# Kernel optimization log

Hardware: AMD Instinct MI355X
Metric: run time of the kernel (lower is better)

The kernel has to match this reference:

```python
import jax, jax.numpy as jnp
import numpy as np
from jax import lax

NUM_CLASSES = 5
NUM_TASKS = 20
CONV_CHANS = [(64, 3), (64, 64), (128, 64), (128, 128), (256, 128), (256, 256)]  # (out, in)


def setup_inputs() -> dict:
    key = jax.random.key(0)
    ks = jax.random.split(key, 16)
    B = 512
    x = jax.random.normal(ks[0], (B, 3, 32, 32), dtype=jnp.float32)
    tid = jax.random.randint(ks[1], (B,), 0, NUM_TASKS)
    inp = {"x": x, "tid": tid}
    for i, (oc, ic) in enumerate(CONV_CHANS):
        fan_in = ic * 9
        inp[f"w{i}"] = jax.random.normal(ks[2 + 2 * i], (oc, ic, 3, 3), dtype=jnp.float32) * np.float32((2.0 / fan_in) ** 0.5)
        inp[f"b{i}"] = jnp.zeros((oc,), dtype=jnp.float32)
    inp["cw"] = jax.random.normal(ks[14], (NUM_CLASSES * NUM_TASKS, 4096), dtype=jnp.float32) * np.float32(4096 ** -0.5)
    inp["cb"] = jnp.zeros((NUM_CLASSES * NUM_TASKS,), dtype=jnp.float32)
    return inp


def _conv_relu(x, w, b):
    y = lax.conv_general_dilated(x, w, window_strides=(1, 1), padding='SAME',
                                 dimension_numbers=('NCHW', 'OIHW', 'NCHW'))
    return jax.nn.relu(y + b[None, :, None, None])


def _maxpool2(x):
    return lax.reduce_window(x, -jnp.inf, lax.max, (1, 1, 2, 2), (1, 1, 2, 2), 'VALID')


def _forward(x, tid, ws, bs, cw, cb):
    # VGG cfg [64,64,'M',128,128,'M',256,256,'M']
    h = _conv_relu(x, ws[0], bs[0])
    h = _conv_relu(h, ws[1], bs[1])
    h = _maxpool2(h)
    h = _conv_relu(h, ws[2], bs[2])
    h = _conv_relu(h, ws[3], bs[3])
    h = _maxpool2(h)
    h = _conv_relu(h, ws[4], bs[4])
    h = _conv_relu(h, ws[5], bs[5])
    h = _maxpool2(h)                      # [B, 256, 4, 4]
    feat = h.reshape(h.shape[0], -1)      # [B, 4096], matches torch NCHW flatten
    # Batched task-indexed classifier: gather each sample's 5-row weight block.
    w_sel = cw.reshape(NUM_TASKS, NUM_CLASSES, 4096)[tid]   # [B, 5, 4096]
    b_sel = cb.reshape(NUM_TASKS, NUM_CLASSES)[tid]         # [B, 5]
    return jnp.einsum('bcd,bd->bc', w_sel, feat) + b_sel


def reference(x, tid, w0, b0, w1, b1, w2, b2, w3, b3, w4, b4, w5, b5, cw, cb):
    ws = (w0, w1, w2, w3, w4, w5)
    bs = (b0, b1, b2, b3, b4, b5)
    return _forward(x, tid, ws, bs, cw, cb)
```

## Files before the change

kernel.cpp:

```cpp
#include <hip/hip_runtime.h>


typedef __attribute__((ext_vector_type(8))) short short8;
typedef __attribute__((ext_vector_type(4))) float floatx4;
typedef unsigned int uint;
typedef unsigned short ushort;

__device__ __forceinline__ ushort f2bf(float f) {
    uint u = __float_as_uint(f);
    return (ushort)((u + 0x7fffu + ((u >> 16) & 1u)) >> 16);
}
__device__ __forceinline__ float bf2f(ushort h) {
    return __uint_as_float(((uint)h) << 16);
}

typedef const __attribute__((address_space(1))) unsigned int* gas_ptr;
typedef __attribute__((address_space(3))) unsigned int* las_ptr;
__device__ __forceinline__ void gload_lds16(const void* g, void* l) {
    __builtin_amdgcn_global_load_lds((gas_ptr)g, (las_ptr)l, 16, 0, 0);
}

__device__ __forceinline__ void wlin_one(
    const float* __restrict__ src, short* __restrict__ dst, int OC, int IC, int o)
{
    int j    = o & 7;
    int lane = (o >> 3) & 63;
    int r    = o >> 9;
    int G16  = OC >> 4;
    int g    = r % G16;  r /= G16;
    int kk   = r % 9;
    int icb  = r / 9;
    int oc = g * 16 + (lane & 15);
    int ic = icb * 32 + (lane >> 4) * 8 + j;
    dst[o] = (short)f2bf(src[((long)oc * IC + ic) * 9 + kk]);
}

#define N_W0 2048
#define N_W1 36864
#define N_W2 73728
#define N_W3 147456
#define N_W4 294912
#define N_W5 589824
#define N_CWB (100 * 4096)
#define N_WT_TOTAL (N_W0 + N_W1 + N_W2 + N_W3 + N_W4 + N_W5)
#define N_ALL (N_WT_TOTAL + N_CWB)

__global__ __launch_bounds__(256) void wtransform_all(
    const float* __restrict__ w0, const float* __restrict__ w1,
    const float* __restrict__ w2, const float* __restrict__ w3,
    const float* __restrict__ w4, const float* __restrict__ w5,
    const float* __restrict__ cw,
    short* __restrict__ wt0, short* __restrict__ wts1, short* __restrict__ wts2,
    short* __restrict__ wts3, short* __restrict__ wts4, short* __restrict__ wts5,
    short* __restrict__ zp, short* __restrict__ cwb)
{
    if (blockIdx.x == 0 && threadIdx.x < 32) zp[threadIdx.x] = 0;
    int idx = blockIdx.x * 256 + threadIdx.x;
    if (idx < N_W0) {
        int oc = idx >> 5, k = idx & 31;
        wt0[idx] = (k < 27) ? (short)f2bf(w0[oc * 27 + k]) : (short)0;
        return;
    }
    idx -= N_W0;
    if (idx < N_W1) { wlin_one(w1, wts1, 64, 64, idx); return; }
    idx -= N_W1;
    if (idx < N_W2) { wlin_one(w2, wts2, 128, 64, idx); return; }
    idx -= N_W2;
    if (idx < N_W3) { wlin_one(w3, wts3, 128, 128, idx); return; }
    idx -= N_W3;
    if (idx < N_W4) { wlin_one(w4, wts4, 256, 128, idx); return; }
    idx -= N_W4;
    if (idx < N_W5) { wlin_one(w5, wts5, 256, 256, idx); return; }
    idx -= N_W5;
    if (idx < N_CWB) cwb[idx] = (short)f2bf(cw[idx]);
}

__global__ __launch_bounds__(256, 2) void conv0_mfma(
    const float* __restrict__ x, const short* __restrict__ wT0,
    const float* __restrict__ b0, ushort* __restrict__ out)
{
    __shared__ float  s_x[3 * 18 * 34];
    __shared__ ushort s_b[4 * 512 * 8];

    const int tid  = threadIdx.x;
    const int wv   = tid >> 6;
    const int lane = tid & 63;
    const int quad = lane >> 4;
    const int l16  = lane & 15;
    const int b    = blockIdx.x >> 1;
    const int r0   = (blockIdx.x & 1) * 16;

    for (int idx = tid; idx < 3 * 18 * 34; idx += 256) {
        int c   = idx / 612;
        int rem = idx - c * 612;
        int ry  = rem / 34, rx = rem - ry * 34;
        int gy  = r0 + ry - 1, gx = rx - 1;
        float v = 0.f;
        if (gy >= 0 && gy < 32 && gx >= 0 && gx < 32)
            v = x[(((long)b * 3 + c) * 32 + gy) * 32 + gx];
        s_x[idx] = v;
    }
    __syncthreads();

#pragma unroll
    for (int rep = 0; rep < 2; ++rep) {
        int pxl = rep * 256 + tid;
        int py = pxl >> 5, px = pxl & 31;
        ushort v[32];
#pragma unroll
        for (int c = 0; c < 3; ++c)
#pragma unroll
            for (int ky = 0; ky < 3; ++ky)
#pragma unroll
                for (int kx = 0; kx < 3; ++kx)
                    v[c * 9 + ky * 3 + kx] = f2bf(s_x[c * 612 + (py + ky) * 34 + (px + kx)]);
#pragma unroll
        for (int k = 27; k < 32; ++k) v[k] = 0;
#pragma unroll
        for (int q = 0; q < 4; ++q)
            *(uint4*)(&s_b[(q * 512 + pxl) * 8]) = *(const uint4*)(v + q * 8);
    }
    __syncthreads();

    floatx4 acc[4][8];
#pragma unroll
    for (int i = 0; i < 4; ++i)
#pragma unroll
        for (int t = 0; t < 8; ++t) acc[i][t] = (floatx4)0.f;

    short8 afr[4];
#pragma unroll
    for (int i = 0; i < 4; ++i)
        afr[i] = *(const short8*)(wT0 + (i * 16 + l16) * 32 + quad * 8);
#pragma unroll
    for (int t = 0; t < 8; ++t) {
        int pxl = wv * 128 + t * 16 + l16;
        short8 bfr = *(const short8*)(&s_b[(quad * 512 + pxl) * 8]);
#pragma unroll
        for (int i = 0; i < 4; ++i)
            acc[i][t] = __builtin_amdgcn_mfma_f32_16x16x32_bf16(afr[i], bfr, acc[i][t], 0, 0, 0);
    }

#pragma unroll
    for (int i = 0; i < 4; ++i) {
        int oc0 = i * 16 + quad * 4;
        float4 bv = *(const float4*)(b0 + oc0);
#pragma unroll
        for (int t = 0; t < 8; ++t) {
            int pxl = wv * 128 + t * 16 + l16;
            int py = pxl >> 5, px = pxl & 31;
            long dst = ((((long)b * 8 + (oc0 >> 3)) * 32 + r0 + py) * 32 + px) * 8 + (oc0 & 7);
            float v0 = acc[i][t][0] + bv.x;
            float v1 = acc[i][t][1] + bv.y;
            float v2 = acc[i][t][2] + bv.z;
            float v3 = acc[i][t][3] + bv.w;
            ushort o[4];
            o[0] = f2bf(v0 > 0.f ? v0 : 0.f);
            o[1] = f2bf(v1 > 0.f ? v1 : 0.f);
            o[2] = f2bf(v2 > 0.f ? v2 : 0.f);
            o[3] = f2bf(v3 > 0.f ? v3 : 0.f);
            *(uint2*)(out + dst) = *(uint2*)o;
        }
    }
}

template<int IC, int OC, int H, int W, int ROWS, int OCGROUPS, bool POOL>
__global__ __launch_bounds__(256, 3) void conv_so(
    const ushort* __restrict__ act_in,
    const short*  __restrict__ wTs,
    const float*  __restrict__ bias,
    ushort* __restrict__ act_out,
    const ushort* __restrict__ zp)
{
    constexpr int WPAD  = W + 2;
    constexpr int RPAD  = ROWS + 2;
    constexpr int UNITS = RPAD * WPAD;
    constexpr int UNITSP = UNITS + 2;
    constexpr int SEGS  = H / ROWS;
    constexpr int C8I   = IC / 8;
    constexpr int G16   = OC / 16;
    constexpr int NICB  = IC / 32;
    constexpr int C8O   = OC / 8;
    constexpr int TMAX  = NICB * 9;
    constexpr int NSTG  = UNITSP * C8I;

    __shared__ ushort s_act[NSTG * 8];

    const int tid  = threadIdx.x;
    const int wv   = tid >> 6;
    const int lane = tid & 63;
    const int quad = lane >> 4;
    const int l16  = lane & 15;

    const int b   = blockIdx.x / SEGS;
    const int seg = blockIdx.x - b * SEGS;
    const int r0  = seg * ROWS;
    const int ocg = wv % OCGROUPS;
    const int pxg = wv / OCGROUPS;

    for (int c = tid; c < NSTG; c += 256) {
        int sub  = c / UNITSP;
        int unit = c - sub * UNITSP;
        int ry   = unit / WPAD, cx = unit - ry * WPAD;
        int gy   = r0 + ry - 1, gx = cx - 1;
        const ushort* src = zp;
        if (unit < UNITS && (unsigned)gy < (unsigned)H && (unsigned)gx < (unsigned)W)
            src = act_in + ((((long)b * C8I + sub) * H + gy) * W + gx) * 8;
        gload_lds16(src, &s_act[(size_t)(c - lane) * 8]);
    }
    __syncthreads();

    floatx4 acc[4][4];
#pragma unroll
    for (int i = 0; i < 4; ++i)
#pragma unroll
        for (int t = 0; t < 4; ++t) acc[i][t] = (floatx4)0.f;

    int bbase[4];
#pragma unroll
    for (int t = 0; t < 4; ++t) {
        int pxl = pxg * 64 + t * 16 + l16;
        int py  = pxl / W, px = pxl - py * W;
        bbase[t] = (py * WPAD + px) * 8;
    }

    const short8* wb = (const short8*)wTs;
    const int  wbase = (ocg * 4) * 64 + lane;
    const long WSTEP = (long)G16 * 64;

    short8 wpipe[3][4];
#pragma unroll
    for (int d = 0; d < 3; ++d)
#pragma unroll
        for (int i = 0; i < 4; ++i)
            wpipe[d][i] = wb[(long)d * WSTEP + wbase + i * 64];

    int tl = 0;
    for (int icb = 0; icb < NICB; ++icb) {
#pragma unroll
        for (int kk = 0; kk < 9; ++kk) {
            const int ky = kk / 3, kx = kk - ky * 3;
            const int koff = ((icb * 4 + quad) * UNITSP + ky * WPAD + kx) * 8;
            short8 bfr[4];
#pragma unroll
            for (int t = 0; t < 4; ++t)
                bfr[t] = *(const short8*)(&s_act[bbase[t] + koff]);
            const int slot = kk % 3;
#pragma unroll
            for (int i = 0; i < 4; ++i)
#pragma unroll
                for (int t = 0; t < 4; ++t)
                    acc[i][t] = __builtin_amdgcn_mfma_f32_16x16x32_bf16(
                        wpipe[slot][i], bfr[t], acc[i][t], 0, 0, 0);
            int tn = tl + 3;
            if (tn >= TMAX) tn = 0;
#pragma unroll
            for (int i = 0; i < 4; ++i)
                wpipe[slot][i] = wb[(long)tn * WSTEP + wbase + i * 64];
            ++tl;
        }
    }

    if constexpr (!POOL) {
#pragma unroll
        for (int i = 0; i < 4; ++i) {
            int oc0 = ocg * 64 + i * 16 + quad * 4;
            float4 bv = *(const float4*)(bias + oc0);
#pragma unroll
            for (int t = 0; t < 4; ++t) {
                int pxl = pxg * 64 + t * 16 + l16;
                int py  = pxl / W, px = pxl - py * W;
                long dst = ((((long)b * C8O + (oc0 >> 3)) * H + r0 + py) * W + px) * 8 + (oc0 & 7);
                float v0 = acc[i][t][0] + bv.x;
                float v1 = acc[i][t][1] + bv.y;
                float v2 = acc[i][t][2] + bv.z;
                float v3 = acc[i][t][3] + bv.w;
                ushort o[4];
                o[0] = f2bf(v0 > 0.f ? v0 : 0.f);
                o[1] = f2bf(v1 > 0.f ? v1 : 0.f);
                o[2] = f2bf(v2 > 0.f ? v2 : 0.f);
                o[3] = f2bf(v3 > 0.f ? v3 : 0.f);
                *(uint2*)(act_out + dst) = *(uint2*)o;
            }
        }
    } else {
        __syncthreads();
        ushort* s_pool = s_act;
        constexpr int PSTR = OC + 8;
        static_assert(ROWS * W * PSTR <= NSTG * 8, "pool scratch fits");
#pragma unroll
        for (int i = 0; i < 4; ++i) {
            int oc0 = ocg * 64 + i * 16 + quad * 4;
            float4 bv = *(const float4*)(bias + oc0);
#pragma unroll
            for (int t = 0; t < 4; ++t) {
                int pxl = pxg * 64 + t * 16 + l16;
                float v0 = acc[i][t][0] + bv.x;
                float v1 = acc[i][t][1] + bv.y;
                float v2 = acc[i][t][2] + bv.z;
                float v3 = acc[i][t][3] + bv.w;
                ushort o[4];
                o[0] = f2bf(v0 > 0.f ? v0 : 0.f);
                o[1] = f2bf(v1 > 0.f ? v1 : 0.f);
                o[2] = f2bf(v2 > 0.f ? v2 : 0.f);
                o[3] = f2bf(v3 > 0.f ? v3 : 0.f);
                *(uint2*)(&s_pool[pxl * PSTR + oc0]) = *(uint2*)o;
            }
        }
        __syncthreads();
        constexpr int PH = ROWS / 2, PW = W / 2, HOT = H / 2;
        const int pr0 = r0 / 2;
        for (int u = tid; u < PH * PW * C8O; u += 256) {
            int c8 = u % C8O;
            int pp = u / C8O;
            int xo = pp % PW, yo = pp / PW;
            const ushort* p00 = &s_pool[((2 * yo) * W + 2 * xo) * PSTR + c8 * 8];
            uint4 q0 = *(const uint4*)(p00);
            uint4 q1 = *(const uint4*)(p00 + PSTR);
            uint4 q2 = *(const uint4*)(p00 + W * PSTR);
            uint4 q3 = *(const uint4*)(p00 + W * PSTR + PSTR);
            const ushort* a0 = (const ushort*)&q0;
            const ushort* a1 = (const ushort*)&q1;
            const ushort* a2 = (const ushort*)&q2;
            const ushort* a3 = (const ushort*)&q3;
            ushort r[8];
#pragma unroll
            for (int j = 0; j < 8; ++j) {
                ushort m0 = a0[j] > a1[j] ? a0[j] : a1[j];
                ushort m1 = a2[j] > a3[j] ? a2[j] : a3[j];
                r[j] = m0 > m1 ? m0 : m1;
            }
            long dst = ((((long)b * C8O + c8) * HOT + pr0 + yo) * PW + xo) * 8;
            *(uint4*)(act_out + dst) = *(uint4*)r;
        }
    }
}

template<int IC, int OC, bool POOL, bool CLS>
__global__ __launch_bounds__(256, 1) void conv_so2i(
    const ushort* __restrict__ act_in,
    const short*  __restrict__ wTs,
    const float*  __restrict__ bias,
    ushort* __restrict__ act_out,
    const ushort* __restrict__ zp,
    const int*   __restrict__ tids,
    const short* __restrict__ cwb,
    const float* __restrict__ cbv,
    float*       __restrict__ outp)
{
    constexpr int H = 8, W = 8;
    constexpr int WPAD  = 10;
    constexpr int UNITS = 100;
    constexpr int UNITSP = 102;
    constexpr int C8I   = IC / 8;
    constexpr int G16   = OC / 16;
    constexpr int NICB  = IC / 32;
    constexpr int C8O   = OC / 8;
    constexpr int TMAX  = NICB * 9;
    constexpr int NSTG  = UNITSP * C8I;

    __shared__ ushort s_act[2 * NSTG * 8];

    const int tid  = threadIdx.x;
    const int wv   = tid >> 6;
    const int lane = tid & 63;
    const int quad = lane >> 4;
    const int l16  = lane & 15;
    const int ocg  = wv;
    const long b0i = (long)blockIdx.x * 2;

    for (int c = tid; c < 2 * NSTG; c += 256) {
        int img  = c / NSTG;
        int cc   = c - img * NSTG;
        int sub  = cc / UNITSP;
        int unit = cc - sub * UNITSP;
        int ry   = unit / WPAD, cx = unit - ry * WPAD;
        int gy   = ry - 1, gx = cx - 1;
        const ushort* src = zp;
        if (unit < UNITS && (unsigned)gy < (unsigned)H && (unsigned)gx < (unsigned)W)
            src = act_in + ((((b0i + img) * C8I + sub) * H + gy) * W + gx) * 8;
        gload_lds16(src, &s_act[(size_t)(c - lane) * 8]);
    }
    __syncthreads();

    floatx4 acc[4][2][4];
#pragma unroll
    for (int i = 0; i < 4; ++i)
#pragma unroll
        for (int g = 0; g < 2; ++g)
#pragma unroll
            for (int t = 0; t < 4; ++t) acc[i][g][t] = (floatx4)0.f;

    int bbase[2][4];
#pragma unroll
    for (int g = 0; g < 2; ++g)
#pragma unroll
        for (int t = 0; t < 4; ++t) {
            int pxl = t * 16 + l16;
            int py  = pxl >> 3, px = pxl & 7;
            bbase[g][t] = (py * WPAD + px) * 8 + g * NSTG * 8;
        }

    const short8* wb = (const short8*)wTs;
    const int  wbase = (ocg * 4) * 64 + lane;
    const long WSTEP = (long)G16 * 64;

    short8 wpipe[3][4];
#pragma unroll
    for (int d = 0; d < 3; ++d)
#pragma unroll
        for (int i = 0; i < 4; ++i)
            wpipe[d][i] = wb[(long)d * WSTEP + wbase + i * 64];

    int tl = 0;
    for (int icb = 0; icb < NICB; ++icb) {
#pragma unroll
        for (int kk = 0; kk < 9; ++kk) {
            const int ky = kk / 3, kx = kk - ky * 3;
            const int koff = ((icb * 4 + quad) * UNITSP + ky * WPAD + kx) * 8;
            short8 bfr[2][4];
#pragma unroll
            for (int g = 0; g < 2; ++g)
#pragma unroll
                for (int t = 0; t < 4; ++t)
                    bfr[g][t] = *(const short8*)(&s_act[bbase[g][t] + koff]);
            const int slot = kk % 3;
#pragma unroll
            for (int i = 0; i < 4; ++i)
#pragma unroll
                for (int g = 0; g < 2; ++g)
#pragma unroll
                    for (int t = 0; t < 4; ++t)
                        acc[i][g][t] = __builtin_amdgcn_mfma_f32_16x16x32_bf16(
                            wpipe[slot][i], bfr[g][t], acc[i][g][t], 0, 0, 0);
            int tn = tl + 3;
            if (tn >= TMAX) tn = 0;
#pragma unroll
            for (int i = 0; i < 4; ++i)
                wpipe[slot][i] = wb[(long)tn * WSTEP + wbase + i * 64];
            ++tl;
        }
    }

    if constexpr (!POOL) {
#pragma unroll
        for (int i = 0; i < 4; ++i) {
            int oc0 = ocg * 64 + i * 16 + quad * 4;
            float4 bv = *(const float4*)(bias + oc0);
#pragma unroll
            for (int g = 0; g < 2; ++g)
#pragma unroll
                for (int t = 0; t < 4; ++t) {
                    int pxl = t * 16 + l16;
                    int py  = pxl >> 3, px = pxl & 7;
                    long dst = ((((b0i + g) * C8O + (oc0 >> 3)) * H + py) * W + px) * 8 + (oc0 & 7);
                    float v0 = acc[i][g][t][0] + bv.x;
                    float v1 = acc[i][g][t][1] + bv.y;
                    float v2 = acc[i][g][t][2] + bv.z;
                    float v3 = acc[i][g][t][3] + bv.w;
                    ushort o[4];
                    o[0] = f2bf(v0 > 0.f ? v0 : 0.f);
                    o[1] = f2bf(v1 > 0.f ? v1 : 0.f);
                    o[2] = f2bf(v2 > 0.f ? v2 : 0.f);
                    o[3] = f2bf(v3 > 0.f ? v3 : 0.f);
                    *(uint2*)(act_out + dst) = *(uint2*)o;
                }
        }
    } else {
        __syncthreads();
        ushort* s_pool = s_act;
        constexpr int PSTR = OC + 8;
        static_assert(H * W * PSTR <= NSTG * 8, "pool scratch fits per image");
        static_assert(!CLS || (2 * NSTG * 8 - 8192 >= NSTG * 8 + H * W * PSTR), "s_feat fits");
#pragma unroll
        for (int i = 0; i < 4; ++i) {
            int oc0 = ocg * 64 + i * 16 + quad * 4;
            float4 bv = *(const float4*)(bias + oc0);
#pragma unroll
            for (int g = 0; g < 2; ++g)
#pragma unroll
                for (int t = 0; t < 4; ++t) {
                    int pxl = t * 16 + l16;
                    float v0 = acc[i][g][t][0] + bv.x;
                    float v1 = acc[i][g][t][1] + bv.y;
                    float v2 = acc[i][g][t][2] + bv.z;
                    float v3 = acc[i][g][t][3] + bv.w;
                    ushort o[4];
                    o[0] = f2bf(v0 > 0.f ? v0 : 0.f);
                    o[1] = f2bf(v1 > 0.f ? v1 : 0.f);
                    o[2] = f2bf(v2 > 0.f ? v2 : 0.f);
                    o[3] = f2bf(v3 > 0.f ? v3 : 0.f);
                    *(uint2*)(&s_pool[(size_t)g * NSTG * 8 + pxl * PSTR + oc0]) = *(uint2*)o;
                }
        }
        __syncthreads();
        constexpr int PH = 4, PW = 4, HOT = 4;
        ushort* s_feat = s_act + (2 * NSTG * 8 - 8192);
        for (int u = tid; u < 2 * PH * PW * C8O; u += 256) {
            int img = u / (PH * PW * C8O);
            int uu  = u - img * (PH * PW * C8O);
            int c8 = uu % C8O;
            int pp = uu / C8O;
            int xo = pp % PW, yo = pp / PW;
            const ushort* p00 = &s_pool[(size_t)img * NSTG * 8 + ((2 * yo) * W + 2 * xo) * PSTR + c8 * 8];
            uint4 q0 = *(const uint4*)(p00);
            uint4 q1 = *(const uint4*)(p00 + PSTR);
            uint4 q2 = *(const uint4*)(p00 + W * PSTR);
            uint4 q3 = *(const uint4*)(p00 + W * PSTR + PSTR);
            const ushort* a0 = (const ushort*)&q0;
            const ushort* a1 = (const ushort*)&q1;
            const ushort* a2 = (const ushort*)&q2;
            const ushort* a3 = (const ushort*)&q3;
            ushort r[8];
#pragma unroll
            for (int j = 0; j < 8; ++j) {
                ushort m0 = a0[j] > a1[j] ? a0[j] : a1[j];
                ushort m1 = a2[j] > a3[j] ? a2[j] : a3[j];
                r[j] = m0 > m1 ? m0 : m1;
            }
            if constexpr (CLS) {
#pragma unroll
                for (int j = 0; j < 8; ++j)
                    s_feat[img * 4096 + (c8 * 8 + j) * 16 + pp] = r[j];
            } else {
                long dst = ((((b0i + img) * C8O + c8) * HOT + yo) * PW + xo) * 8;
                *(uint4*)(act_out + dst) = *(uint4*)r;
            }
        }
        if constexpr (CLS) {
            __syncthreads();
            const int t0 = tids[b0i], t1 = tids[b0i + 1];
            for (int u = wv; u < 10; u += 4) {
                int img = u & 1, c = u >> 1;
                int t = img ? t1 : t0;
                const short* wrow = cwb + (long)(t * 5 + c) * 4096;
                const ushort* f = s_feat + img * 4096;
                float s = 0.f;
#pragma unroll
                for (int j = 0; j < 8; ++j) {
                    short8 wv8 = *(const short8*)(wrow + lane * 8 + 512 * j);
                    short8 fv8 = *(const short8*)(f + lane * 8 + 512 * j);
#pragma unroll
                    for (int e = 0; e < 8; ++e)
                        s += bf2f((ushort)wv8[e]) * bf2f((ushort)fv8[e]);
                }
#pragma unroll
                for (int off = 32; off > 0; off >>= 1) s += __shfl_down(s, off, 64);
                if (lane == 0) outp[(b0i + img) * 5 + c] = s + cbv[t * 5 + c];
            }
        }
    }
}

extern "C" void kernel_launch(void* const* d_in, const int* in_sizes, int n_in,
                              void* d_out, int out_size, void* d_ws, size_t ws_size,
                              hipStream_t stream)
{
    const float* x   = (const float*)d_in[0];
    const int*   tid = (const int*)d_in[1];
    const float* w0 = (const float*)d_in[2];  const float* b0 = (const float*)d_in[3];
    const float* w1 = (const float*)d_in[4];  const float* b1 = (const float*)d_in[5];
    const float* w2 = (const float*)d_in[6];  const float* b2 = (const float*)d_in[7];
    const float* w3 = (const float*)d_in[8];  const float* b3 = (const float*)d_in[9];
    const float* w4 = (const float*)d_in[10]; const float* b4 = (const float*)d_in[11];
    const float* w5 = (const float*)d_in[12]; const float* b5 = (const float*)d_in[13];
    const float* cw = (const float*)d_in[14];
    const float* cb = (const float*)d_in[15];
    float* outp = (float*)d_out;

    const int B = in_sizes[0] / (3 * 32 * 32);

    short* wt0  = (short*)d_ws;
    short* wts1 = wt0 + N_W0;
    short* wts2 = wts1 + N_W1;
    short* wts3 = wts2 + N_W2;
    short* wts4 = wts3 + N_W3;
    short* wts5 = wts4 + N_W4;
    short* zp   = wts5 + N_W5;
    short* cwb  = zp + 32;
    const size_t WT_HW = (size_t)N_WT_TOTAL + 32 + N_CWB;
    const size_t fixed_bytes = WT_HW * 2;

    int Bc = B;
    while (Bc > 2 && fixed_bytes + (size_t)Bc * 2 * 65536 * 2 > ws_size) Bc >>= 1;
    if (Bc < 2) Bc = 2;

    ushort* bufA = (ushort*)((short*)d_ws + WT_HW);
    ushort* bufB = bufA + (size_t)Bc * 65536;

    wtransform_all<<<(N_ALL + 255) / 256, 256, 0, stream>>>(
        w0, w1, w2, w3, w4, w5, cw,
        wt0, wts1, wts2, wts3, wts4, wts5, zp, cwb);

    for (int cb0 = 0; cb0 < B; cb0 += Bc) {
        const float* xc = x + (size_t)cb0 * 3 * 32 * 32;
        const int* tidc = tid + cb0;
        float* outc = outp + (size_t)cb0 * 5;

        conv0_mfma<<<Bc * 2, 256, 0, stream>>>(xc, wt0, b0, bufA);
        conv_so<64, 64, 32, 32, 8, 1, true><<<Bc * 4, 256, 0, stream>>>(
            bufA, wts1, b1, bufB, (ushort*)zp);
        conv_so<64, 128, 16, 16, 8, 2, false><<<Bc * 2, 256, 0, stream>>>(
            bufB, wts2, b2, bufA, (ushort*)zp);
        conv_so<128, 128, 16, 16, 8, 2, true><<<Bc * 2, 256, 0, stream>>>(
            bufA, wts3, b3, bufB, (ushort*)zp);
        conv_so2i<128, 256, false, false><<<Bc / 2, 256, 0, stream>>>(
            bufB, wts4, b4, bufA, (ushort*)zp, nullptr, nullptr, nullptr, nullptr);
        conv_so2i<256, 256, true, true><<<Bc / 2, 256, 0, stream>>>(
            bufA, wts5, b5, bufB, (ushort*)zp, tidc, cwb, cb, outc);
    }
}
```

Measured before the change: 318.9 us.

## Fuse conv4, conv5, pool and classifier into one per-image kernel

Replaces the two 2-image conv_so2i launches with a single kernel per image that runs conv4 into a zero-padded LDS buffer, then conv5, pooling and the task classifier, so the conv4 activation never goes to global memory. The classifier weights are permuted at transform time to match a channel-contiguous feature layout in LDS, and the dot product is split across all four waves with an LDS reduction. Launch bounds move to 2 blocks per CU with one image per block. In exchange, each block now re-reads the full conv4 and conv5 weights for a single image rather than sharing them across two, which doubles weight traffic per image.

```diff
diff --git a/kernel.cpp b/kernel.cpp
--- a/kernel.cpp
+++ b/kernel.cpp
@@ -72,7 +72,15 @@
     idx -= N_W4;
     if (idx < N_W5) { wlin_one(w5, wts5, 256, 256, idx); return; }
     idx -= N_W5;
-    if (idx < N_CWB) cwb[idx] = (short)f2bf(cw[idx]);
+    if (idx < N_CWB) {
+        int row = idx >> 12;
+        int m   = idx & 4095;
+        int pp  = m >> 8;
+        int c8  = (m >> 3) & 31;
+        int j   = m & 7;
+        int d   = (c8 * 8 + j) * 16 + pp;
+        cwb[idx] = (short)f2bf(cw[(long)row * 4096 + d]);
+    }
 }
 
 __global__ __launch_bounds__(256, 2) void conv0_mfma(
@@ -336,30 +344,27 @@
     }
 }
 
-template<int IC, int OC, bool POOL, bool CLS>
-__global__ __launch_bounds__(256, 1) void conv_so2i(
+__global__ __launch_bounds__(256, 2) void conv45_cls(
     const ushort* __restrict__ act_in,
-    const short*  __restrict__ wTs,
-    const float*  __restrict__ bias,
-    ushort* __restrict__ act_out,
+    const short*  __restrict__ wts4,
+    const float*  __restrict__ b4v,
+    const short*  __restrict__ wts5,
+    const float*  __restrict__ b5v,
     const ushort* __restrict__ zp,
-    const int*   __restrict__ tids,
-    const short* __restrict__ cwb,
-    const float* __restrict__ cbv,
-    float*       __restrict__ outp)
+    const int*    __restrict__ tids,
+    const short*  __restrict__ cwb,
+    const float*  __restrict__ cbv,
+    float*        __restrict__ outp)
 {
-    constexpr int H = 8, W = 8;
-    constexpr int WPAD  = 10;
-    constexpr int UNITS = 100;
-    constexpr int UNITSP = 102;
-    constexpr int C8I   = IC / 8;
-    constexpr int G16   = OC / 16;
-    constexpr int NICB  = IC / 32;
-    constexpr int C8O   = OC / 8;
-    constexpr int TMAX  = NICB * 9;
-    constexpr int NSTG  = UNITSP * C8I;
-
-    __shared__ ushort s_act[2 * NSTG * 8];
+    constexpr int WPAD = 10, UNITS = 100, UNITSP = 102;
+    constexpr int C8I  = 16;
+    constexpr int C8M  = 32;
+    constexpr int NSTG = UNITSP * C8I;
+    constexpr int NMID = UNITSP * C8M;
+    constexpr int PSTR = 264;
+
+    __shared__ ushort s_in[NSTG * 8];
+    __shared__ ushort s_mid[NMID * 8];
 
     const int tid  = threadIdx.x;
     const int wv   = tid >> 6;
@@ -367,188 +372,207 @@
     const int quad = lane >> 4;
     const int l16  = lane & 15;
     const int ocg  = wv;
-    const long b0i = (long)blockIdx.x * 2;
-
-    for (int c = tid; c < 2 * NSTG; c += 256) {
-        int img  = c / NSTG;
-        int cc   = c - img * NSTG;
-        int sub  = cc / UNITSP;
-        int unit = cc - sub * UNITSP;
+    const long b   = blockIdx.x;
+
+    for (int c = tid; c < NSTG; c += 256) {
+        int sub  = c / UNITSP;
+        int unit = c - sub * UNITSP;
         int ry   = unit / WPAD, cx = unit - ry * WPAD;
         int gy   = ry - 1, gx = cx - 1;
         const ushort* src = zp;
-        if (unit < UNITS && (unsigned)gy < (unsigned)H && (unsigned)gx < (unsigned)W)
-            src = act_in + ((((b0i + img) * C8I + sub) * H + gy) * W + gx) * 8;
-        gload_lds16(src, &s_act[(size_t)(c - lane) * 8]);
-    }
-    __syncthreads();
-
-    floatx4 acc[4][2][4];
-#pragma unroll
-    for (int i = 0; i < 4; ++i)
-#pragma unroll
-        for (int g = 0; g < 2; ++g)
-#pragma unroll
-            for (int t = 0; t < 4; ++t) acc[i][g][t] = (floatx4)0.f;
-
-    int bbase[2][4];
-#pragma unroll
-    for (int g = 0; g < 2; ++g)
+        if (unit < UNITS && (unsigned)gy < 8u && (unsigned)gx < 8u)
+            src = act_in + (((b * C8I + sub) * 8 + gy) * 8 + gx) * 8;
+        gload_lds16(src, &s_in[(size_t)(c - lane) * 8]);
+    }
+    for (int c = tid; c < NMID; c += 256)
+        *(uint4*)(&s_mid[(size_t)c * 8]) = make_uint4(0, 0, 0, 0);
+    __syncthreads();
+
+    int bbase[4];
+#pragma unroll
+    for (int t = 0; t < 4; ++t) {
+        int pxl = t * 16 + l16;
+        int py  = pxl >> 3, px = pxl & 7;
+        bbase[t] = (py * WPAD + px) * 8;
+    }
+
+    const int  wbase = (ocg * 4) * 64 + lane;
+    const long WSTEP = (long)16 * 64;
+
+    floatx4 acc[4][4];
+    short8 wpipe[3][4];
+
+    {
+#pragma unroll
+        for (int i = 0; i < 4; ++i)
+#pragma unroll
+            for (int t = 0; t < 4; ++t) acc[i][t] = (floatx4)0.f;
+        const short8* wb = (const short8*)wts4;
+#pragma unroll
+        for (int d = 0; d < 3; ++d)
+#pragma unroll
+            for (int i = 0; i < 4; ++i)
+                wpipe[d][i] = wb[(long)d * WSTEP + wbase + i * 64];
+        int tl = 0;
+        for (int icb = 0; icb < 4; ++icb) {
+#pragma unroll
+            for (int kk = 0; kk < 9; ++kk) {
+                const int ky = kk / 3, kx = kk - ky * 3;
+                const int koff = ((icb * 4 + quad) * UNITSP + ky * WPAD + kx) * 8;
+                short8 bfr[4];
+#pragma unroll
+                for (int t = 0; t < 4; ++t)
+                    bfr[t] = *(const short8*)(&s_in[bbase[t] + koff]);
+                const int slot = kk % 3;
+#pragma unroll
+                for (int i = 0; i < 4; ++i)
+#pragma unroll
+                    for (int t = 0; t < 4; ++t)
+                        acc[i][t] = __builtin_amdgcn_mfma_f32_16x16x32_bf16(
+                            wpipe[slot][i], bfr[t], acc[i][t], 0, 0, 0);
+                int tn = tl + 3;
+                if (tn >= 36) tn = 0;
+#pragma unroll
+                for (int i = 0; i < 4; ++i)
+                    wpipe[slot][i] = wb[(long)tn * WSTEP + wbase + i * 64];
+                ++tl;
+            }
+        }
+#pragma unroll
+        for (int i = 0; i < 4; ++i) {
+            int oc0 = ocg * 64 + i * 16 + quad * 4;
+            float4 bv = *(const float4*)(b4v + oc0);
+#pragma unroll
+            for (int t = 0; t < 4; ++t) {
+                int pxl = t * 16 + l16;
+                int py  = pxl >> 3, px = pxl & 7;
+                int unit = (py + 1) * WPAD + (px + 1);
+                float v0 = acc[i][t][0] + bv.x;
+                float v1 = acc[i][t][1] + bv.y;
+                float v2 = acc[i][t][2] + bv.z;
+                float v3 = acc[i][t][3] + bv.w;
+                ushort o[4];
+                o[0] = f2bf(v0 > 0.f ? v0 : 0.f);
+                o[1] = f2bf(v1 > 0.f ? v1 : 0.f);
+                o[2] = f2bf(v2 > 0.f ? v2 : 0.f);
+                o[3] = f2bf(v3 > 0.f ? v3 : 0.f);
+                *(uint2*)(&s_mid[((size_t)(oc0 >> 3) * UNITSP + unit) * 8 + (oc0 & 7)]) = *(uint2*)o;
+            }
+        }
+    }
+    __syncthreads();
+
+    {
+#pragma unroll
+        for (int i = 0; i < 4; ++i)
+#pragma unroll
+            for (int t = 0; t < 4; ++t) acc[i][t] = (floatx4)0.f;
+        const short8* wb = (const short8*)wts5;
+#pragma unroll
+        for (int d = 0; d < 3; ++d)
+#pragma unroll
+            for (int i = 0; i < 4; ++i)
+                wpipe[d][i] = wb[(long)d * WSTEP + wbase + i * 64];
+        int tl = 0;
+        for (int icb = 0; icb < 8; ++icb) {
+#pragma unroll
+            for (int kk = 0; kk < 9; ++kk) {
+                const int ky = kk / 3, kx = kk - ky * 3;
+                const int koff = ((icb * 4 + quad) * UNITSP + ky * WPAD + kx) * 8;
+                short8 bfr[4];
+#pragma unroll
+                for (int t = 0; t < 4; ++t)
+                    bfr[t] = *(const short8*)(&s_mid[bbase[t] + koff]);
+                const int slot = kk % 3;
+#pragma unroll
+                for (int i = 0; i < 4; ++i)
+#pragma unroll
+                    for (int t = 0; t < 4; ++t)
+                        acc[i][t] = __builtin_amdgcn_mfma_f32_16x16x32_bf16(
+                            wpipe[slot][i], bfr[t], acc[i][t], 0, 0, 0);
+                int tn = tl + 3;
+                if (tn >= 72) tn = 0;
+#pragma unroll
+                for (int i = 0; i < 4; ++i)
+                    wpipe[slot][i] = wb[(long)tn * WSTEP + wbase + i * 64];
+                ++tl;
+            }
+        }
+    }
+    __syncthreads();
+
+    ushort* s_pool = s_mid;
+#pragma unroll
+    for (int i = 0; i < 4; ++i) {
+        int oc0 = ocg * 64 + i * 16 + quad * 4;
+        float4 bv = *(const float4*)(b5v + oc0);
 #pragma unroll
         for (int t = 0; t < 4; ++t) {
             int pxl = t * 16 + l16;
-            int py  = pxl >> 3, px = pxl & 7;
-            bbase[g][t] = (py * WPAD + px) * 8 + g * NSTG * 8;
-        }
-
-    const short8* wb = (const short8*)wTs;
-    const int  wbase = (ocg * 4) * 64 + lane;
-    const long WSTEP = (long)G16 * 64;
-
-    short8 wpipe[3][4];
-#pragma unroll
-    for (int d = 0; d < 3; ++d)
-#pragma unroll
-        for (int i = 0; i < 4; ++i)
-            wpipe[d][i] = wb[(long)d * WSTEP + wbase + i * 64];
-
-    int tl = 0;
-    for (int icb = 0; icb < NICB; ++icb) {
-#pragma unroll
-        for (int kk = 0; kk < 9; ++kk) {
-            const int ky = kk / 3, kx = kk - ky * 3;
-            const int koff = ((icb * 4 + quad) * UNITSP + ky * WPAD + kx) * 8;
-            short8 bfr[2][4];
-#pragma unroll
-            for (int g = 0; g < 2; ++g)
-#pragma unroll
-                for (int t = 0; t < 4; ++t)
-                    bfr[g][t] = *(const short8*)(&s_act[bbase[g][t] + koff]);
-            const int slot = kk % 3;
-#pragma unroll
-            for (int i = 0; i < 4; ++i)
-#pragma unroll
-                for (int g = 0; g < 2; ++g)
-#pragma unroll
-                    for (int t = 0; t < 4; ++t)
-                        acc[i][g][t] = __builtin_amdgcn_mfma_f32_16x16x32_bf16(
-                            wpipe[slot][i], bfr[g][t], acc[i][g][t], 0, 0, 0);
-            int tn = tl + 3;
-            if (tn >= TMAX) tn = 0;
-#pragma unroll
-            for (int i = 0; i < 4; ++i)
-                wpipe[slot][i] = wb[(long)tn * WSTEP + wbase + i * 64];
-            ++tl;
-        }
-    }
-
-    if constexpr (!POOL) {
-#pragma unroll
-        for (int i = 0; i < 4; ++i) {
-            int oc0 = ocg * 64 + i * 16 + quad * 4;
-            float4 bv = *(const float4*)(bias + oc0);
-#pragma unroll
-            for (int g = 0; g < 2; ++g)
-#pragma unroll
-                for (int t = 0; t < 4; ++t) {
-                    int pxl = t * 16 + l16;
-                    int py  = pxl >> 3, px = pxl & 7;
-                    long dst = ((((b0i + g) * C8O + (oc0 >> 3)) * H + py) * W + px) * 8 + (oc0 & 7);
-                    float v0 = acc[i][g][t][0] + bv.x;
-                    float v1 = acc[i][g][t][1] + bv.y;
-                    float v2 = acc[i][g][t][2] + bv.z;
-                    float v3 = acc[i][g][t][3] + bv.w;
-                    ushort o[4];
-                    o[0] = f2bf(v0 > 0.f ? v0 : 0.f);
-                    o[1] = f2bf(v1 > 0.f ? v1 : 0.f);
-                    o[2] = f2bf(v2 > 0.f ? v2 : 0.f);
-                    o[3] = f2bf(v3 > 0.f ? v3 : 0.f);
-                    *(uint2*)(act_out + dst) = *(uint2*)o;
-                }
-        }
-    } else {
-        __syncthreads();
-        ushort* s_pool = s_act;
-        constexpr int PSTR = OC + 8;
-        static_assert(H * W * PSTR <= NSTG * 8, "pool scratch fits per image");
-        static_assert(!CLS || (2 * NSTG * 8 - 8192 >= NSTG * 8 + H * W * PSTR), "s_feat fits");
-#pragma unroll
-        for (int i = 0; i < 4; ++i) {
-            int oc0 = ocg * 64 + i * 16 + quad * 4;
-            float4 bv = *(const float4*)(bias + oc0);
-#pragma unroll
-            for (int g = 0; g < 2; ++g)
-#pragma unroll
-                for (int t = 0; t < 4; ++t) {
-                    int pxl = t * 16 + l16;
-                    float v0 = acc[i][g][t][0] + bv.x;
-                    float v1 = acc[i][g][t][1] + bv.y;
-                    float v2 = acc[i][g][t][2] + bv.z;
-                    float v3 = acc[i][g][t][3] + bv.w;
-                    ushort o[4];
-                    o[0] = f2bf(v0 > 0.f ? v0 : 0.f);
-                    o[1] = f2bf(v1 > 0.f ? v1 : 0.f);
-                    o[2] = f2bf(v2 > 0.f ? v2 : 0.f);
-                    o[3] = f2bf(v3 > 0.f ? v3 : 0.f);
-                    *(uint2*)(&s_pool[(size_t)g * NSTG * 8 + pxl * PSTR + oc0]) = *(uint2*)o;
-                }
-        }
-        __syncthreads();
-        constexpr int PH = 4, PW = 4, HOT = 4;
-        ushort* s_feat = s_act + (2 * NSTG * 8 - 8192);
-        for (int u = tid; u < 2 * PH * PW * C8O; u += 256) {
-            int img = u / (PH * PW * C8O);
-            int uu  = u - img * (PH * PW * C8O);
-            int c8 = uu % C8O;
-            int pp = uu / C8O;
-            int xo = pp % PW, yo = pp / PW;
-            const ushort* p00 = &s_pool[(size_t)img * NSTG * 8 + ((2 * yo) * W + 2 * xo) * PSTR + c8 * 8];
-            uint4 q0 = *(const uint4*)(p00);
-            uint4 q1 = *(const uint4*)(p00 + PSTR);
-            uint4 q2 = *(const uint4*)(p00 + W * PSTR);
-            uint4 q3 = *(const uint4*)(p00 + W * PSTR + PSTR);
-            const ushort* a0 = (const ushort*)&q0;
-            const ushort* a1 = (const ushort*)&q1;
-            const ushort* a2 = (const ushort*)&q2;
-            const ushort* a3 = (const ushort*)&q3;
-            ushort r[8];
-#pragma unroll
-            for (int j = 0; j < 8; ++j) {
-                ushort m0 = a0[j] > a1[j] ? a0[j] : a1[j];
-                ushort m1 = a2[j] > a3[j] ? a2[j] : a3[j];
-                r[j] = m0 > m1 ? m0 : m1;
-            }
-            if constexpr (CLS) {
-#pragma unroll
-                for (int j = 0; j < 8; ++j)
-                    s_feat[img * 4096 + (c8 * 8 + j) * 16 + pp] = r[j];
-            } else {
-                long dst = ((((b0i + img) * C8O + c8) * HOT + yo) * PW + xo) * 8;
-                *(uint4*)(act_out + dst) = *(uint4*)r;
-            }
-        }
-        if constexpr (CLS) {
-            __syncthreads();
-            const int t0 = tids[b0i], t1 = tids[b0i + 1];
-            for (int u = wv; u < 10; u += 4) {
-                int img = u & 1, c = u >> 1;
-                int t = img ? t1 : t0;
-                const short* wrow = cwb + (long)(t * 5 + c) * 4096;
-                const ushort* f = s_feat + img * 4096;
-                float s = 0.f;
-#pragma unroll
-                for (int j = 0; j < 8; ++j) {
-                    short8 wv8 = *(const short8*)(wrow + lane * 8 + 512 * j);
-                    short8 fv8 = *(const short8*)(f + lane * 8 + 512 * j);
-#pragma unroll
-                    for (int e = 0; e < 8; ++e)
-                        s += bf2f((ushort)wv8[e]) * bf2f((ushort)fv8[e]);
-                }
-#pragma unroll
-                for (int off = 32; off > 0; off >>= 1) s += __shfl_down(s, off, 64);
-                if (lane == 0) outp[(b0i + img) * 5 + c] = s + cbv[t * 5 + c];
-            }
-        }
+            float v0 = acc[i][t][0] + bv.x;
+            float v1 = acc[i][t][1] + bv.y;
+            float v2 = acc[i][t][2] + bv.z;
+            float v3 = acc[i][t][3] + bv.w;
+            ushort o[4];
+            o[0] = f2bf(v0 > 0.f ? v0 : 0.f);
+            o[1] = f2bf(v1 > 0.f ? v1 : 0.f);
+            o[2] = f2bf(v2 > 0.f ? v2 : 0.f);
+            o[3] = f2bf(v3 > 0.f ? v3 : 0.f);
+            *(uint2*)(&s_pool[pxl * PSTR + oc0]) = *(uint2*)o;
+        }
+    }
+    __syncthreads();
+
+    ushort* s_feat = s_in;
+    float*  s_red  = (float*)(s_in + 4096);
+    for (int u = tid; u < 512; u += 256) {
+        int c8 = u & 31;
+        int pp = u >> 5;
+        int xo = pp & 3, yo = pp >> 2;
+        const ushort* p00 = &s_pool[((2 * yo) * 8 + 2 * xo) * PSTR + c8 * 8];
+        uint4 q0 = *(const uint4*)(p00);
+        uint4 q1 = *(const uint4*)(p00 + PSTR);
+        uint4 q2 = *(const uint4*)(p00 + 8 * PSTR);
+        uint4 q3 = *(const uint4*)(p00 + 8 * PSTR + PSTR);
+        const ushort* a0 = (const ushort*)&q0;
+        const ushort* a1 = (const ushort*)&q1;
+        const ushort* a2 = (const ushort*)&q2;
+        const ushort* a3 = (const ushort*)&q3;
+        ushort r[8];
+#pragma unroll
+        for (int j = 0; j < 8; ++j) {
+            ushort m0 = a0[j] > a1[j] ? a0[j] : a1[j];
+            ushort m1 = a2[j] > a3[j] ? a2[j] : a3[j];
+            r[j] = m0 > m1 ? m0 : m1;
+        }
+        *(uint4*)(&s_feat[(size_t)u * 8]) = *(uint4*)r;
+    }
+    __syncthreads();
+
+    const int t = tids[b];
+    const short* cbase = cwb + (long)t * 5 * 4096;
+#pragma unroll
+    for (int c = 0; c < 5; ++c) {
+        const short*  wrow = cbase + (long)c * 4096 + wv * 1024 + lane * 16;
+        const ushort* fr   = s_feat + wv * 1024 + lane * 16;
+        short8 w0 = *(const short8*)(wrow);
+        short8 w1 = *(const short8*)(wrow + 8);
+        short8 f0 = *(const short8*)(fr);
+        short8 f1 = *(const short8*)(fr + 8);
+        float s = 0.f;
+#pragma unroll
+        for (int e = 0; e < 8; ++e) {
+            s += bf2f((ushort)w0[e]) * bf2f((ushort)f0[e]);
+            s += bf2f((ushort)w1[e]) * bf2f((ushort)f1[e]);
+        }
+#pragma unroll
+        for (int off = 32; off > 0; off >>= 1) s += __shfl_down(s, off, 64);
+        if (lane == 0) s_red[c * 4 + wv] = s;
+    }
+    __syncthreads();
+    if (tid < 5) {
+        float s = s_red[tid * 4] + s_red[tid * 4 + 1] + s_red[tid * 4 + 2] + s_red[tid * 4 + 3];
+        outp[b * 5 + tid] = s + cbv[t * 5 + tid];
     }
 }
 
@@ -604,9 +628,7 @@
             bufB, wts2, b2, bufA, (ushort*)zp);
         conv_so<128, 128, 16, 16, 8, 2, true><<<Bc * 2, 256, 0, stream>>>(
             bufA, wts3, b3, bufB, (ushort*)zp);
-        conv_so2i<128, 256, false, false><<<Bc / 2, 256, 0, stream>>>(
-            bufB, wts4, b4, bufA, (ushort*)zp, nullptr, nullptr, nullptr, nullptr);
-        conv_so2i<256, 256, true, true><<<Bc / 2, 256, 0, stream>>>(
-            bufA, wts5, b5, bufB, (ushort*)zp, tidc, cwb, cb, outc);
-    }
-}
+        conv45_cls<<<Bc, 256, 0, stream>>>(
+            bufB, wts4, b4, wts5, b5, (ushort*)zp, tidc, cwb, cb, outc);
+    }
+}
```

Result: faster. 301.1 us (-5.6%).
